# Kernel tuning notes

Hardware: AMD Instinct MI355X
Metric: run time of the kernel (lower is better)

Reference implementation:

```python
import jax, jax.numpy as jnp
import numpy as np
from jax import lax

B, C, H, W = 128, 512, 10, 20
MD, S2 = 20, 2  # max_displacement, stride2 -> 21x21 = 441 displacements


def setup_inputs() -> dict:
    key = jax.random.key(0)
    ks = jax.random.split(key, 26)
    rn = lambda k, s, sc: jax.random.normal(k, s, jnp.float32) * sc
    z = lambda s: jnp.zeros(s, jnp.float32)
    return {
        "feat1": rn(ks[0], (B, C, H, W), 1.0),
        "feat2": rn(ks[1], (B, C, H, W), 1.0),
        "feat3": rn(ks[2], (B, C, H, W), 1.0),
        # 1x1 input convs
        "Wa": rn(ks[3], (512, 512), 0.001), "ba": z(512),
        "Wb": rn(ks[4], (512, 512), 0.001), "bb": z(512),
        "Wc": rn(ks[5], (512, 512), 0.001), "bc": z(512),
        # corr head 3x3 conv: 441*3 -> 3
        "Wcorr": rn(ks[6], (3, 1323, 3, 3), 0.001), "bcorr": z(3),
        # concat head 3x3 conv: 1536 -> 3
        "Wcat": rn(ks[7], (3, 1536, 3, 3), 0.001), "bcat": z(3),
        # corr_feat MLP 600->256->128
        "cf_w1": rn(ks[8], (256, 600), 0.01), "cf_b1": z(256),
        "cf_w2": rn(ks[9], (128, 256), 0.01), "cf_b2": z(128),
        # concat_feat MLP 600->256->128
        "ccf_w1": rn(ks[10], (256, 600), 0.01), "ccf_b1": z(256),
        "ccf_w2": rn(ks[11], (128, 256), 0.01), "ccf_b2": z(128),
        # final linear 256->2
        "Wout": rn(ks[12], (2, 256), 0.01), "bout": z(2),
    }


def _conv1x1(x, w, b):
    return jnp.einsum('bchw,oc->bohw', x, w) + b[None, :, None, None]


def _conv3x3(x, w, b):
    y = lax.conv_general_dilated(x, w, (1, 1), 'SAME',
                                 dimension_numbers=('NCHW', 'OIHW', 'NCHW'))
    return y + b[None, :, None, None]


def _correlation(f1, f2):
    # FlowNetC-style cost volume: pad_size=20, kernel_size=1,
    # max_displacement=20, stride1=1, stride2=2 -> 21x21=441 channels,
    # normalized by C (kernel_size^2 * C with kernel_size=1).
    p = jnp.pad(f2, ((0, 0), (0, 0), (MD, MD), (MD, MD)))
    outs = []
    for dy in range(0, 2 * MD + 1, S2):
        for dx in range(0, 2 * MD + 1, S2):
            outs.append(jnp.sum(f1 * p[:, :, dy:dy + H, dx:dx + W], axis=1))
    return jnp.stack(outs, axis=1) / f1.shape[1]  # [B, 441, H, W]


def reference(feat1, feat2, feat3, Wa, ba, Wb, bb, Wc, bc,
              Wcorr, bcorr, Wcat, bcat,
              cf_w1, cf_b1, cf_w2, cf_b2,
              ccf_w1, ccf_b1, ccf_w2, ccf_b2, Wout, bout):
    f1 = _conv1x1(feat1, Wa, ba)
    f2 = _conv1x1(feat2, Wb, bb)
    f3 = _conv1x1(feat3, Wc, bc)

    corr = jnp.concatenate([_correlation(f1, f2),
                            _correlation(f1, f3),
                            _correlation(f2, f3)], axis=1)  # [B,1323,H,W]
    corr = jax.nn.leaky_relu(corr, 0.1)
    corr = jax.nn.relu(_conv3x3(corr, Wcorr, bcorr))  # [B,3,H,W]
    corr = corr.reshape(corr.shape[0], -1)            # [B,600]
    corr = jax.nn.relu(corr @ cf_w1.T + cf_b1)
    corr = jax.nn.relu(corr @ cf_w2.T + cf_b2)        # [B,128]

    cat = jnp.concatenate([f1, f2, f3], axis=1)       # [B,1536,H,W]
    cat = _conv3x3(cat, Wcat, bcat)                   # [B,3,H,W] (no relu, per source)
    cat = cat.reshape(cat.shape[0], -1)               # [B,600]
    cat = jax.nn.relu(cat @ ccf_w1.T + ccf_b1)
    cat = jax.nn.relu(cat @ ccf_w2.T + ccf_b2)        # [B,128]

    out = jnp.concatenate([corr, cat], axis=1)        # [B,256]
    return out @ Wout.T + bout                        # [B,2]
```

## Files before the change

### kernel.cpp

```cpp
#include <hip/hip_runtime.h>
#include <stdint.h>

#define NB 128
#define NC 512
#define NH 10
#define NW 20
#define NP 200
#define ND3 1323
#define NDP 448
#define MROWS 25600
#define KCORR 1344
#define KCAT  1536

typedef unsigned short u16;
typedef unsigned int u32;

typedef short bh8 __attribute__((ext_vector_type(8)));
typedef float f4 __attribute__((ext_vector_type(4)));

#define OFF_FA     0ULL
#define SZ_FA      (3ULL*MROWS*NC*2)
#define OFF_CORR   0ULL
#define SZ_CORR    (3ULL*NB*NP*NDP*2)
#define OFF_UCORR  (OFF_CORR + SZ_CORR + 256)
#define SZ_U       (1ULL*MROWS*32*4)
#define OFF_UCAT   (OFF_UCORR + SZ_U)
#define OFF_FT     (OFF_FA + SZ_FA)
#define SZ_FT      (3ULL*MROWS*NC*2 + 65536)
#define OFF_WBF    (OFF_FT + SZ_FT)
#define SZ_WBF     (3ULL*NC*NC*2)
#define OFF_WCTB   (OFF_WBF + SZ_WBF)
#define SZ_WCTB    (32ULL*KCORR*2)
#define OFF_WCATB  (OFF_WCTB + SZ_WCTB)
#define SZ_WCATB   (32ULL*KCAT*2)

__device__ __forceinline__ float bf2f(u16 a) {
    return __uint_as_float(((u32)a) << 16);
}
__device__ __forceinline__ u16 f2bf(float x) {
    u32 u = __float_as_uint(x);
    return (u16)((u + 0x7fffu + ((u >> 16) & 1u)) >> 16);
}

__device__ __forceinline__ void gload16(const void* g, void* l) {
    __builtin_amdgcn_global_load_lds(
        (const __attribute__((address_space(1))) void*)g,
        (__attribute__((address_space(3))) void*)l, 16, 0, 0);
}

__global__ __launch_bounds__(256) void k_prep(const float* __restrict__ Wcorr,
                                              const float* __restrict__ Wcat,
                                              const float* __restrict__ Wa,
                                              const float* __restrict__ Wb,
                                              const float* __restrict__ Wc,
                                              u16* __restrict__ wctb,
                                              u16* __restrict__ wcatb,
                                              u16* __restrict__ wbf) {
    int idx = blockIdx.x * 256 + threadIdx.x;
    const int n1 = 32 * KCORR;
    const int n2 = 32 * KCAT;
    const int n3 = 3 * NC * NC;
    if (idx < n1) {
        int k = idx % KCORR;
        int n = idx / KCORR;
        int pair = k / NDP, ch = k - pair * NDP;
        float v = 0.0f;
        if (n < 27 && ch < 441) {
            int d = pair * 441 + ch;
            int tap = n / 3, o = n % 3;
            int ky = tap / 3, kx = tap % 3;
            v = Wcorr[((o * ND3 + d) * 3 + ky) * 3 + kx];
        }
        wctb[idx] = f2bf(v);
    } else if (idx < n1 + n2) {
        int j = idx - n1;
        int i = j % KCAT;
        int n = j / KCAT;
        float v = 0.0f;
        if (n < 27) {
            int tap = n / 3, o = n % 3;
            int ky = tap / 3, kx = tap % 3;
            v = Wcat[((o * 1536 + i) * 3 + ky) * 3 + kx];
        }
        wcatb[j] = f2bf(v);
    } else if (idx < n1 + n2 + n3) {
        int j = idx - n1 - n2;
        int t = j >> 18;
        const float* W = (t == 0) ? Wa : (t == 1) ? Wb : Wc;
        wbf[j] = f2bf(W[j & 262143]);
    }
}

__global__ __launch_bounds__(256) void k_fa(const float* __restrict__ feat1,
                                            const float* __restrict__ feat2,
                                            const float* __restrict__ feat3,
                                            u16* __restrict__ fa) {
    const int tid = threadIdx.x;
    const int ct = blockIdx.x;
    const int t = blockIdx.y >> 7, b = blockIdx.y & 127;
    const float* feat = (t == 0) ? feat1 : (t == 1) ? feat2 : feat3;

    __shared__ u16 Ls[NP * 72];

    const int cl = tid >> 2;
    const int pc = tid & 3;
    const float* src = feat + ((size_t)b * NC + ct * 64 + cl) * NP + pc * 50;
#pragma unroll
    for (int u = 0; u < 50; u += 2) {
        float2 v = *(const float2*)(src + u);
        int p = pc * 50 + u;
        Ls[p * 72 + cl] = f2bf(v.x);
        Ls[(p + 1) * 72 + cl] = f2bf(v.y);
    }
    __syncthreads();
    for (int idx = tid; idx < 1600; idx += 256) {
        int p = idx >> 3, ck = idx & 7;
        uint4 v = *(const uint4*)&Ls[p * 72 + ck * 8];
        *(uint4*)&fa[((size_t)t * MROWS + b * NP + p) * NC + ct * 64 + ck * 8] = v;
    }
}

__global__ __launch_bounds__(256) void k_conv1x1_mfma(
    const u16* __restrict__ fa, const u16* __restrict__ wbf,
    const float* __restrict__ ba, const float* __restrict__ bb,
    const float* __restrict__ bc, u16* __restrict__ fT) {
    const int tid = threadIdx.x;
    const int bid = blockIdx.x;
    const int xcd = bid & 7, local = bid >> 3;
    const int mb = xcd * 25 + local / 12;
    const int nbt = local % 12;
    const int nb = nbt & 3;
    const int t = nbt >> 2;
    const float* bias = (t == 0) ? ba : (t == 1) ? bb : bc;

    __shared__ __align__(16) u16 smem[17408];

    const u16* Ag = fa + (size_t)t * MROWS * NC + (size_t)mb * 128 * NC;
    const u16* Bg = wbf + (size_t)t * NC * NC + (size_t)nb * 128 * NC;

    const int lane = tid & 63;
    const int wave = tid >> 6;
    const int wm = (wave & 1) * 64;
    const int wn = (wave >> 1) * 64;
    const int quad = lane >> 4;
    const int ln16 = lane & 15;

    const int r0 = lane >> 3;
    const int csrc = (lane & 7) ^ r0;

    f4 acc[4][4];
    const f4 zz = {0.f, 0.f, 0.f, 0.f};
#pragma unroll
    for (int i = 0; i < 4; ++i)
#pragma unroll
        for (int j = 0; j < 4; ++j) acc[i][j] = zz;

#define STAGE1(ks) do {                                                        \
        int _ko = (ks) * 64 + csrc * 8;                                        \
        _Pragma("unroll")                                                      \
        for (int _i = 0; _i < 4; ++_i) {                                       \
            int _ra = wave * 32 + _i * 8;                                      \
            gload16(Ag + (size_t)(_ra + r0) * NC + _ko, &smem[_ra * 64]);      \
            gload16(Bg + (size_t)(_ra + r0) * NC + _ko,                        \
                    &smem[8192 + _ra * 64]);                                   \
        }                                                                      \
    } while (0)

#pragma unroll
    for (int ks = 0; ks < 8; ++ks) {
        __syncthreads();
        STAGE1(ks);
        __syncthreads();
#pragma unroll
        for (int h = 0; h < 2; ++h) {
            bh8 afr[4], bfr[4];
#pragma unroll
            for (int s = 0; s < 4; ++s) {
                int cw = ((h * 4 + quad) ^ (ln16 & 7)) * 8;
                afr[s] = *(const bh8*)&smem[(wm + s * 16 + ln16) * 64 + cw];
                bfr[s] = *(const bh8*)&smem[8192 + (wn + s * 16 + ln16) * 64 + cw];
            }
#pragma unroll
            for (int i = 0; i < 4; ++i)
#pragma unroll
                for (int j = 0; j < 4; ++j)
                    acc[i][j] = __builtin_amdgcn_mfma_f32_16x16x32_bf16(
                        afr[i], bfr[j], acc[i][j], 0, 0, 0);
        }
    }
#undef STAGE1

    __syncthreads();
#pragma unroll
    for (int j = 0; j < 4; ++j) {
        int tcol = wn + j * 16 + ln16;
        float bi = bias[nb * 128 + tcol];
#pragma unroll
        for (int i = 0; i < 4; ++i) {
            int trow = wm + i * 16 + quad * 4;
#pragma unroll
            for (int r = 0; r < 4; ++r)
                smem[(trow + r) * 136 + tcol] = f2bf(acc[i][j][r] + bi);
        }
    }
    __syncthreads();
    const size_t obase = ((size_t)t * MROWS + (size_t)mb * 128) * NC + nb * 128;
#pragma unroll
    for (int it = 0; it < 8; ++it) {
        int idx = tid + 256 * it;
        int row = idx >> 4, ck = idx & 15;
        *(uint4*)(fT + obase + (size_t)row * NC + ck * 8) =
            *(const uint4*)&smem[row * 136 + ck * 8];
    }
}

__global__ __launch_bounds__(256) void k_gram_mfma(const u16* __restrict__ fT,
                                                   u16* __restrict__ corr) {
    const int tid = threadIdx.x;
    const int bid = blockIdx.x;
    const int xcd = bid & 7, local = bid >> 3;
    const int gidx = xcd * 48 + (local >> 2);
    const int mt = local & 3;
    const int b = gidx / 3, pair = gidx % 3;
    const int tA = (pair == 2) ? 1 : 0;
    const int tB = (pair == 0) ? 1 : 2;

    __shared__ __align__(16) u16 smem[20480];

    const u16* Ag = fT + ((size_t)tA * NB + b) * NP * NC + (size_t)mt * 64 * NC;
    const u16* Bg = fT + ((size_t)tB * NB + b) * NP * NC;

    const int lane = tid & 63;
    const int wave = tid >> 6;
    const int wn = wave * 64;
    const int quad = lane >> 4;
    const int ln16 = lane & 15;

    const int r0 = lane >> 3;
    const int csrc = (lane & 7) ^ r0;

    f4 acc[4][4];
    const f4 zz = {0.f, 0.f, 0.f, 0.f};
#pragma unroll
    for (int i = 0; i < 4; ++i)
#pragma unroll
        for (int j = 0; j < 4; ++j) acc[i][j] = zz;

#define STAGE2(ks) do {                                                        \
        int _ko = (ks) * 64 + csrc * 8;                                        \
        _Pragma("unroll")                                                      \
        for (int _i = 0; _i < 2; ++_i) {                                       \
            int _ra = wave * 16 + _i * 8;                                      \
            gload16(Ag + (size_t)(_ra + r0) * NC + _ko, &smem[_ra * 64]);      \
        }                                                                      \
        _Pragma("unroll")                                                      \
        for (int _i = 0; _i < 8; ++_i) {                                       \
            int _rb = wave * 64 + _i * 8;                                      \
            gload16(Bg + (size_t)(_rb + r0) * NC + _ko,                        \
                    &smem[4096 + _rb * 64]);                                   \
        }                                                                      \
    } while (0)

#pragma unroll
    for (int ks = 0; ks < 8; ++ks) {
        __syncthreads();
        STAGE2(ks);
        __syncthreads();
#pragma unroll
        for (int h = 0; h < 2; ++h) {
            bh8 afr[4], bfr[4];
#pragma unroll
            for (int s = 0; s < 4; ++s) {
                int cw = ((h * 4 + quad) ^ (ln16 & 7)) * 8;
                afr[s] = *(const bh8*)&smem[(s * 16 + ln16) * 64 + cw];
                bfr[s] = *(const bh8*)&smem[4096 + (wn + s * 16 + ln16) * 64 + cw];
            }
#pragma unroll
            for (int i = 0; i < 4; ++i)
#pragma unroll
                for (int j = 0; j < 4; ++j)
                    acc[i][j] = __builtin_amdgcn_mfma_f32_16x16x32_bf16(
                        afr[i], bfr[j], acc[i][j], 0, 0, 0);
        }
    }
#undef STAGE2

    u16* Crow = corr + ((size_t)(b * 3 + pair)) * NP * NDP;
#pragma unroll
    for (int half = 0; half < 2; ++half) {
        __syncthreads();
        {
            const uint4 z4 = make_uint4(0, 0, 0, 0);
#pragma unroll
            for (int it = 0; it < 14; ++it)
                ((uint4*)smem)[tid + 256 * it] = z4;
        }
        __syncthreads();
#pragma unroll
        for (int i = half * 2; i < half * 2 + 2; ++i) {
#pragma unroll
            for (int r = 0; r < 4; ++r) {
                int p1l = i * 16 + quad * 4 + r;
                int lrow = p1l - half * 32;
                int p1 = mt * 64 + p1l;
                if (p1 >= NP) continue;
                int y1 = p1 / 20, x1 = p1 - y1 * 20;
#pragma unroll
                for (int j = 0; j < 4; ++j) {
                    int p2 = wn + j * 16 + ln16;
                    if (p2 >= NP) continue;
                    int y2 = p2 / 20, x2 = p2 - y2 * 20;
                    int oy = y2 - y1, ox = x2 - x1;
                    if (((oy | ox) & 1) == 0) {
                        int ch = ((oy + 20) >> 1) * 21 + ((ox + 20) >> 1);
                        float v = acc[i][j][r] * (1.0f / 512.0f);
                        v = (v > 0.0f) ? v : 0.1f * v;
                        smem[lrow * NDP + ch] = f2bf(v);
                    }
                }
            }
        }
        __syncthreads();
#pragma unroll
        for (int it = 0; it < 7; ++it) {
            int idx = tid + 256 * it;
            int row = idx / 56, cq = idx - row * 56;
            int p1 = mt * 64 + half * 32 + row;
            if (p1 < NP)
                *(uint4*)(Crow + (size_t)p1 * NDP + cq * 8) =
                    *(const uint4*)&smem[row * NDP + cq * 8];
        }
    }
}

#define LDA 72
__global__ __launch_bounds__(256) void k_convgemm(const u16* __restrict__ corr,
                                                  const u16* __restrict__ fT,
                                                  const u16* __restrict__ wctb,
                                                  const u16* __restrict__ wcatb,
                                                  float* __restrict__ Ucorr,
                                                  float* __restrict__ Ucat) {
    const int tid = threadIdx.x;
    const int mb = blockIdx.x;
    const int mode = blockIdx.y;
    const u16* A0 = mode ? fT : corr;
    const u16* Bn = mode ? wcatb : wctb;
    float* U = mode ? Ucat : Ucorr;
    const int kiters = mode ? (KCAT / 64) : (KCORR / 64);
    const int Kpad = kiters * 64;

    __shared__ __align__(16) u16 As[128 * LDA];
    __shared__ __align__(16) u16 Bs[32 * LDA];

    const int lane = tid & 63;
    const int wave = tid >> 6;
    const int wm = wave * 32;
    const int quad = lane >> 4;
    const int ln16 = lane & 15;

    size_t abase[4];
    int ack[4];
#pragma unroll
    for (int i = 0; i < 4; ++i) {
        int idx = tid + 256 * i;
        int r = idx >> 3;
        ack[i] = (idx & 7) * 8;
        int m = mb * 128 + r;
        if (mode == 0) {
            int b = m / NP, p = m - b * NP;
            abase[i] = ((size_t)(b * 3) * NP + p) * NDP;
        } else {
            abase[i] = (size_t)m * NC;
        }
    }

    f4 acc00 = {0,0,0,0}, acc01 = {0,0,0,0}, acc10 = {0,0,0,0}, acc11 = {0,0,0,0};

    uint4 ga[4], gb1;
#pragma unroll
    for (int i = 0; i < 4; ++i) {
        int k = ack[i];
        const u16* ap = (mode == 0)
            ? (A0 + abase[i] + (size_t)(k / NDP) * (NP * NDP) + (k % NDP))
            : (A0 + (size_t)(k >> 9) * MROWS * NC + abase[i] + (k & 511));
        ga[i] = *(const uint4*)ap;
    }
    {
        int r = tid >> 3, ck = tid & 7;
        gb1 = *(const uint4*)(Bn + (size_t)r * Kpad + ck * 8);
    }
    for (int ks = 0; ks < kiters; ++ks) {
        __syncthreads();
#pragma unroll
        for (int i = 0; i < 4; ++i) {
            int idx = tid + 256 * i;
            int r = idx >> 3, ck = idx & 7;
            *(uint4*)&As[r * LDA + ck * 8] = ga[i];
        }
        {
            int r = tid >> 3, ck = tid & 7;
            *(uint4*)&Bs[r * LDA + ck * 8] = gb1;
        }
        __syncthreads();
        if (ks < kiters - 1) {
            int kof = (ks + 1) * 64;
#pragma unroll
            for (int i = 0; i < 4; ++i) {
                int k = kof + ack[i];
                const u16* ap = (mode == 0)
                    ? (A0 + abase[i] + (size_t)(k / NDP) * (NP * NDP) + (k % NDP))
                    : (A0 + (size_t)(k >> 9) * MROWS * NC + abase[i] + (k & 511));
                ga[i] = *(const uint4*)ap;
            }
            int r = tid >> 3, ck = tid & 7;
            gb1 = *(const uint4*)(Bn + (size_t)r * Kpad + kof + ck * 8);
        }
#pragma unroll
        for (int h = 0; h < 2; ++h) {
            bh8 a0 = *(const bh8*)&As[(wm + ln16) * LDA + h * 32 + quad * 8];
            bh8 a1 = *(const bh8*)&As[(wm + 16 + ln16) * LDA + h * 32 + quad * 8];
            bh8 b0 = *(const bh8*)&Bs[(ln16) * LDA + h * 32 + quad * 8];
            bh8 b1 = *(const bh8*)&Bs[(16 + ln16) * LDA + h * 32 + quad * 8];
            acc00 = __builtin_amdgcn_mfma_f32_16x16x32_bf16(a0, b0, acc00, 0, 0, 0);
            acc01 = __builtin_amdgcn_mfma_f32_16x16x32_bf16(a0, b1, acc01, 0, 0, 0);
            acc10 = __builtin_amdgcn_mfma_f32_16x16x32_bf16(a1, b0, acc10, 0, 0, 0);
            acc11 = __builtin_amdgcn_mfma_f32_16x16x32_bf16(a1, b1, acc11, 0, 0, 0);
        }
    }
    const int rbase = mb * 128 + wm + quad * 4;
#pragma unroll
    for (int r = 0; r < 4; ++r) {
        U[(size_t)(rbase + r) * 32 + ln16] = acc00[r];
        U[(size_t)(rbase + r) * 32 + 16 + ln16] = acc01[r];
        U[(size_t)(rbase + 16 + r) * 32 + ln16] = acc10[r];
        U[(size_t)(rbase + 16 + r) * 32 + 16 + ln16] = acc11[r];
    }
}

__global__ __launch_bounds__(256) void k_tail(
    const float* __restrict__ Ucorr, const float* __restrict__ Ucat,
    const float* __restrict__ bcorr, const float* __restrict__ bcat,
    const float* __restrict__ cf_w1, const float* __restrict__ cf_b1,
    const float* __restrict__ cf_w2, const float* __restrict__ cf_b2,
    const float* __restrict__ ccf_w1, const float* __restrict__ ccf_b1,
    const float* __restrict__ ccf_w2, const float* __restrict__ ccf_b2,
    const float* __restrict__ Wout, const float* __restrict__ bout,
    float* __restrict__ out) {
    const int tid = threadIdx.x;
    const int b = blockIdx.x;
    __shared__ float Lc[NP][28];
    __shared__ float La[NP][28];
    __shared__ float cv[600], vv[600], h1[256], h2a[128], h2b[128];
    for (int idx = tid; idx < NP * 27; idx += 256) {
        int p = idx / 27, n = idx - p * 27;
        Lc[p][n] = Ucorr[(size_t)(b * NP + p) * 32 + n];
        La[p][n] = Ucat[(size_t)(b * NP + p) * 32 + n];
    }
    __syncthreads();
    for (int idx = tid; idx < 1200; idx += 256) {
        int path = idx / 600;
        int rem = idx - path * 600;
        int o = rem / 200, p = rem - o * 200;
        int y = p / 20, x = p - y * 20;
        float s = (path == 0) ? bcorr[o] : bcat[o];
        for (int ky = 0; ky < 3; ++ky) {
            int yy = y + ky - 1;
            if (yy < 0 || yy >= NH) continue;
            for (int kx = 0; kx < 3; ++kx) {
                int xx = x + kx - 1;
                if (xx < 0 || xx >= NW) continue;
                int n = (ky * 3 + kx) * 3 + o;
                s += (path == 0) ? Lc[yy * 20 + xx][n] : La[yy * 20 + xx][n];
            }
        }
        if (path == 0) cv[rem] = fmaxf(s, 0.0f);
        else           vv[rem] = s;
    }
    __syncthreads();
    {
        float s = cf_b1[tid];
        const float* wr = cf_w1 + (size_t)tid * 600;
        for (int k = 0; k < 600; k += 4) {
            float4 wv = *(const float4*)&wr[k];
            s = fmaf(cv[k], wv.x, s); s = fmaf(cv[k + 1], wv.y, s);
            s = fmaf(cv[k + 2], wv.z, s); s = fmaf(cv[k + 3], wv.w, s);
        }
        h1[tid] = fmaxf(s, 0.0f);
    }
    __syncthreads();
    if (tid < 128) {
        float s = cf_b2[tid];
        const float* wr = cf_w2 + (size_t)tid * 256;
        for (int k = 0; k < 256; k += 4) {
            float4 wv = *(const float4*)&wr[k];
            s = fmaf(h1[k], wv.x, s); s = fmaf(h1[k + 1], wv.y, s);
            s = fmaf(h1[k + 2], wv.z, s); s = fmaf(h1[k + 3], wv.w, s);
        }
        h2a[tid] = fmaxf(s, 0.0f);
    }
    __syncthreads();
    {
        float s = ccf_b1[tid];
        const float* wr = ccf_w1 + (size_t)tid * 600;
        for (int k = 0; k < 600; k += 4) {
            float4 wv = *(const float4*)&wr[k];
            s = fmaf(vv[k], wv.x, s); s = fmaf(vv[k + 1], wv.y, s);
            s = fmaf(vv[k + 2], wv.z, s); s = fmaf(vv[k + 3], wv.w, s);
        }
        h1[tid] = fmaxf(s, 0.0f);
    }
    __syncthreads();
    if (tid < 128) {
        float s = ccf_b2[tid];
        const float* wr = ccf_w2 + (size_t)tid * 256;
        for (int k = 0; k < 256; k += 4) {
            float4 wv = *(const float4*)&wr[k];
            s = fmaf(h1[k], wv.x, s); s = fmaf(h1[k + 1], wv.y, s);
            s = fmaf(h1[k + 2], wv.z, s); s = fmaf(h1[k + 3], wv.w, s);
        }
        h2b[tid] = fmaxf(s, 0.0f);
    }
    __syncthreads();
    if (tid < 2) {
        float s = bout[tid];
        const float* wr = Wout + (size_t)tid * 256;
        for (int k = 0; k < 128; ++k) {
            s = fmaf(h2a[k], wr[k], s);
            s = fmaf(h2b[k], wr[128 + k], s);
        }
        out[(size_t)b * 2 + tid] = s;
    }
}

extern "C" void kernel_launch(void* const* d_in, const int* in_sizes, int n_in,
                              void* d_out, int out_size, void* d_ws, size_t ws_size,
                              hipStream_t stream) {
    const float* feat1  = (const float*)d_in[0];
    const float* feat2  = (const float*)d_in[1];
    const float* feat3  = (const float*)d_in[2];
    const float* Wa     = (const float*)d_in[3];
    const float* ba     = (const float*)d_in[4];
    const float* Wb     = (const float*)d_in[5];
    const float* bb     = (const float*)d_in[6];
    const float* Wc     = (const float*)d_in[7];
    const float* bc     = (const float*)d_in[8];
    const float* Wcorr  = (const float*)d_in[9];
    const float* bcorr  = (const float*)d_in[10];
    const float* Wcat   = (const float*)d_in[11];
    const float* bcat   = (const float*)d_in[12];
    const float* cf_w1  = (const float*)d_in[13];
    const float* cf_b1  = (const float*)d_in[14];
    const float* cf_w2  = (const float*)d_in[15];
    const float* cf_b2  = (const float*)d_in[16];
    const float* ccf_w1 = (const float*)d_in[17];
    const float* ccf_b1 = (const float*)d_in[18];
    const float* ccf_w2 = (const float*)d_in[19];
    const float* ccf_b2 = (const float*)d_in[20];
    const float* Wout   = (const float*)d_in[21];
    const float* bout   = (const float*)d_in[22];

    char* ws = (char*)d_ws;
    u16*  fa    = (u16*)(ws + OFF_FA);
    u16*  corr  = (u16*)(ws + OFF_CORR);
    float* Ucorr = (float*)(ws + OFF_UCORR);
    float* Ucat  = (float*)(ws + OFF_UCAT);
    u16*  fT    = (u16*)(ws + OFF_FT);
    u16*  wbf   = (u16*)(ws + OFF_WBF);
    u16*  wctb  = (u16*)(ws + OFF_WCTB);
    u16*  wcatb = (u16*)(ws + OFF_WCATB);

    k_prep<<<3432, 256, 0, stream>>>(Wcorr, Wcat, Wa, Wb, Wc, wctb, wcatb, wbf);
    k_fa<<<dim3(8, 384), 256, 0, stream>>>(feat1, feat2, feat3, fa);
    k_conv1x1_mfma<<<2400, 256, 0, stream>>>(fa, wbf, ba, bb, bc, fT);
    k_gram_mfma<<<1536, 256, 0, stream>>>(fT, corr);
    k_convgemm<<<dim3(200, 2), 256, 0, stream>>>(corr, fT, wctb, wcatb, Ucorr, Ucat);
    k_tail<<<128, 256, 0, stream>>>(Ucorr, Ucat, bcorr, bcat,
                                    cf_w1, cf_b1, cf_w2, cf_b2,
                                    ccf_w1, ccf_b1, ccf_w2, ccf_b2, Wout, bout,
                                    (float*)d_out);
}
```

Measured before the change: 451.3 us.

## Rewrite convgemm to load MFMA operands directly from global with register double-buffering

The conv-GEMM kernel no longer stages A and B tiles through shared memory with two barriers per k-step. Each wave now owns 16 output rows and loads its MFMA fragments straight from global memory into registers, double-buffered across k-steps. The grid doubles to 400x2 blocks to raise parallelism. In exchange, the B weights are re-read by every wave instead of shared within a block, which leans more on cache bandwidth.

```diff
diff --git a/kernel.cpp b/kernel.cpp
--- a/kernel.cpp
+++ b/kernel.cpp
@@ -333,7 +333,6 @@
     }
 }
 
-#define LDA 72
 __global__ __launch_bounds__(256) void k_convgemm(const u16* __restrict__ corr,
                                                   const u16* __restrict__ fT,
                                                   const u16* __restrict__ wctb,
@@ -341,7 +340,6 @@
                                                   float* __restrict__ Ucorr,
                                                   float* __restrict__ Ucat) {
     const int tid = threadIdx.x;
-    const int mb = blockIdx.x;
     const int mode = blockIdx.y;
     const u16* A0 = mode ? fT : corr;
     const u16* Bn = mode ? wcatb : wctb;
@@ -349,91 +347,72 @@
     const int kiters = mode ? (KCAT / 64) : (KCORR / 64);
     const int Kpad = kiters * 64;
 
-    __shared__ __align__(16) u16 As[128 * LDA];
-    __shared__ __align__(16) u16 Bs[32 * LDA];
-
     const int lane = tid & 63;
     const int wave = tid >> 6;
-    const int wm = wave * 32;
     const int quad = lane >> 4;
     const int ln16 = lane & 15;
-
-    size_t abase[4];
-    int ack[4];
-#pragma unroll
-    for (int i = 0; i < 4; ++i) {
-        int idx = tid + 256 * i;
-        int r = idx >> 3;
-        ack[i] = (idx & 7) * 8;
-        int m = mb * 128 + r;
-        if (mode == 0) {
-            int b = m / NP, p = m - b * NP;
-            abase[i] = ((size_t)(b * 3) * NP + p) * NDP;
-        } else {
-            abase[i] = (size_t)m * NC;
-        }
-    }
-
-    f4 acc00 = {0,0,0,0}, acc01 = {0,0,0,0}, acc10 = {0,0,0,0}, acc11 = {0,0,0,0};
-
-    uint4 ga[4], gb1;
-#pragma unroll
-    for (int i = 0; i < 4; ++i) {
-        int k = ack[i];
-        const u16* ap = (mode == 0)
-            ? (A0 + abase[i] + (size_t)(k / NDP) * (NP * NDP) + (k % NDP))
-            : (A0 + (size_t)(k >> 9) * MROWS * NC + abase[i] + (k & 511));
-        ga[i] = *(const uint4*)ap;
-    }
-    {
-        int r = tid >> 3, ck = tid & 7;
-        gb1 = *(const uint4*)(Bn + (size_t)r * Kpad + ck * 8);
-    }
-    for (int ks = 0; ks < kiters; ++ks) {
-        __syncthreads();
-#pragma unroll
-        for (int i = 0; i < 4; ++i) {
-            int idx = tid + 256 * i;
-            int r = idx >> 3, ck = idx & 7;
-            *(uint4*)&As[r * LDA + ck * 8] = ga[i];
-        }
-        {
-            int r = tid >> 3, ck = tid & 7;
-            *(uint4*)&Bs[r * LDA + ck * 8] = gb1;
-        }
-        __syncthreads();
-        if (ks < kiters - 1) {
-            int kof = (ks + 1) * 64;
-#pragma unroll
-            for (int i = 0; i < 4; ++i) {
-                int k = kof + ack[i];
-                const u16* ap = (mode == 0)
-                    ? (A0 + abase[i] + (size_t)(k / NDP) * (NP * NDP) + (k % NDP))
-                    : (A0 + (size_t)(k >> 9) * MROWS * NC + abase[i] + (k & 511));
-                ga[i] = *(const uint4*)ap;
-            }
-            int r = tid >> 3, ck = tid & 7;
-            gb1 = *(const uint4*)(Bn + (size_t)r * Kpad + kof + ck * 8);
-        }
-#pragma unroll
-        for (int h = 0; h < 2; ++h) {
-            bh8 a0 = *(const bh8*)&As[(wm + ln16) * LDA + h * 32 + quad * 8];
-            bh8 a1 = *(const bh8*)&As[(wm + 16 + ln16) * LDA + h * 32 + quad * 8];
-            bh8 b0 = *(const bh8*)&Bs[(ln16) * LDA + h * 32 + quad * 8];
-            bh8 b1 = *(const bh8*)&Bs[(16 + ln16) * LDA + h * 32 + quad * 8];
-            acc00 = __builtin_amdgcn_mfma_f32_16x16x32_bf16(a0, b0, acc00, 0, 0, 0);
-            acc01 = __builtin_amdgcn_mfma_f32_16x16x32_bf16(a0, b1, acc01, 0, 0, 0);
-            acc10 = __builtin_amdgcn_mfma_f32_16x16x32_bf16(a1, b0, acc10, 0, 0, 0);
-            acc11 = __builtin_amdgcn_mfma_f32_16x16x32_bf16(a1, b1, acc11, 0, 0, 0);
-        }
-    }
-    const int rbase = mb * 128 + wm + quad * 4;
+    const int wbase = (blockIdx.x * 4 + wave) * 16;
+    const int arow = wbase + ln16;
+
+    size_t abase;
+    if (mode == 0) {
+        int b = arow / NP, p = arow - b * NP;
+        abase = ((size_t)(b * 3) * NP + p) * NDP;
+    } else {
+        abase = (size_t)arow * NC;
+    }
+
+    f4 acc0 = {0, 0, 0, 0}, acc1 = {0, 0, 0, 0};
+
+    bh8 pa[2][2], pb0[2][2], pb1[2][2];
+
+#define PFC(buf, ks) do {                                                      \
+        _Pragma("unroll")                                                      \
+        for (int _h = 0; _h < 2; ++_h) {                                       \
+            int _k = (ks) * 64 + _h * 32 + quad * 8;                           \
+            const u16* _ap;                                                    \
+            if (mode == 0) {                                                   \
+                int _pr = _k / NDP;                                            \
+                _ap = A0 + abase + (size_t)_pr * (NP * NDP) + (_k - _pr * NDP);\
+            } else {                                                           \
+                _ap = A0 + (size_t)(_k >> 9) * ((size_t)MROWS * NC) + abase    \
+                      + (_k & 511);                                            \
+            }                                                                  \
+            pa[buf][_h]  = *(const bh8*)_ap;                                   \
+            pb0[buf][_h] = *(const bh8*)(Bn + (size_t)ln16 * Kpad + _k);       \
+            pb1[buf][_h] = *(const bh8*)(Bn + (size_t)(16 + ln16) * Kpad + _k);\
+        }                                                                      \
+    } while (0)
+
+#define CGM(buf) do {                                                          \
+        acc0 = __builtin_amdgcn_mfma_f32_16x16x32_bf16(pa[buf][0],             \
+                   pb0[buf][0], acc0, 0, 0, 0);                                \
+        acc1 = __builtin_amdgcn_mfma_f32_16x16x32_bf16(pa[buf][0],             \
+                   pb1[buf][0], acc1, 0, 0, 0);                                \
+        acc0 = __builtin_amdgcn_mfma_f32_16x16x32_bf16(pa[buf][1],             \
+                   pb0[buf][1], acc0, 0, 0, 0);                                \
+        acc1 = __builtin_amdgcn_mfma_f32_16x16x32_bf16(pa[buf][1],             \
+                   pb1[buf][1], acc1, 0, 0, 0);                                \
+    } while (0)
+
+    PFC(0, 0);
+    PFC(1, 1);
+    int ks = 0;
+    for (; ks + 1 < kiters; ks += 2) {
+        CGM(0);
+        if (ks + 2 < kiters) PFC(0, ks + 2);
+        CGM(1);
+        if (ks + 3 < kiters) PFC(1, ks + 3);
+    }
+    if (ks < kiters) CGM(0);
+#undef PFC
+#undef CGM
+
+    const int orow = wbase + quad * 4;
 #pragma unroll
     for (int r = 0; r < 4; ++r) {
-        U[(size_t)(rbase + r) * 32 + ln16] = acc00[r];
-        U[(size_t)(rbase + r) * 32 + 16 + ln16] = acc01[r];
-        U[(size_t)(rbase + 16 + r) * 32 + ln16] = acc10[r];
-        U[(size_t)(rbase + 16 + r) * 32 + 16 + ln16] = acc11[r];
+        U[(size_t)(orow + r) * 32 + ln16] = acc0[r];
+        U[(size_t)(orow + r) * 32 + 16 + ln16] = acc1[r];
     }
 }
 
@@ -573,7 +552,7 @@
     k_fa<<<dim3(8, 384), 256, 0, stream>>>(feat1, feat2, feat3, fa);
     k_conv1x1_mfma<<<2400, 256, 0, stream>>>(fa, wbf, ba, bb, bc, fT);
     k_gram_mfma<<<1536, 256, 0, stream>>>(fT, corr);
-    k_convgemm<<<dim3(200, 2), 256, 0, stream>>>(corr, fT, wctb, wcatb, Ucorr, Ucat);
+    k_convgemm<<<dim3(400, 2), 256, 0, stream>>>(corr, fT, wctb, wcatb, Ucorr, Ucat);
     k_tail<<<128, 256, 0, stream>>>(Ucorr, Ucat, bcorr, bcat,
                                     cf_w1, cf_b1, cf_w2, cf_b2,
                                     ccf_w1, ccf_b1, ccf_w2, ccf_b2, Wout, bout,
```

Result: no change. 451.0 us (-0.1%).
